# Optimization experiments

Measured on AMD Instinct MI355X. Metric: run time of the kernel, lower is better.

## Reference

```python
import jax, jax.numpy as jnp
import numpy as np

HIDDEN = 768
NUM_HEADS = 12
HEAD_DIM = HIDDEN // NUM_HEADS
BIAS_SCALE = 0.5


def setup_inputs() -> dict:
    key = jax.random.key(0)
    ks = jax.random.split(key, 8)
    B, S = 4, 2048
    s = 1.0 / np.sqrt(HIDDEN)
    return {
        "hidden_states": jax.random.normal(ks[0], (B, S, HIDDEN), dtype=jnp.float32),
        "attention_mask": jnp.ones((B, S), dtype=jnp.float32),
        "Wq": jax.random.normal(ks[1], (HIDDEN, HIDDEN), dtype=jnp.float32) * s,
        "bq": jnp.zeros((HIDDEN,), dtype=jnp.float32),
        "Wk": jax.random.normal(ks[2], (HIDDEN, HIDDEN), dtype=jnp.float32) * s,
        "bk": jnp.zeros((HIDDEN,), dtype=jnp.float32),
        "Wv": jax.random.normal(ks[3], (HIDDEN, HIDDEN), dtype=jnp.float32) * s,
        "bv": jnp.zeros((HIDDEN,), dtype=jnp.float32),
        "head_bias": jnp.full((NUM_HEADS, 1, 1), 0.1, dtype=jnp.float32),
    }


def _split_heads(x):
    # [B,S,H] -> [B,nh,S,hd]
    B, S, _ = x.shape
    return x.reshape(B, S, NUM_HEADS, HEAD_DIM).transpose(0, 2, 1, 3)


def reference(hidden_states, attention_mask, Wq, bq, Wk, bk, Wv, bv, head_bias):
    q = _split_heads(hidden_states @ Wq.T + bq)
    k = _split_heads(hidden_states @ Wk.T + bk)
    v = _split_heads(hidden_states @ Wv.T + bv)
    # [B,nh,S,S]
    scores = jnp.einsum("bhqd,bhkd->bhqk", q, k) / np.sqrt(HEAD_DIM).astype(np.float32)
    scores = scores + BIAS_SCALE * head_bias  # head_bias broadcasts [nh,1,1]
    ext_mask = (1.0 - attention_mask[:, None, None, :]) * -10000.0
    scores = scores + ext_mask
    probs = jax.nn.softmax(scores, axis=-1)  # dropout is identity in eval
    ctx = jnp.einsum("bhqk,bhkd->bhqd", probs, v)
    B, _, S, _ = ctx.shape
    return ctx.transpose(0, 2, 1, 3).reshape(B, S, HIDDEN)
```

## Files before the change

kernel.cpp:

```cpp
#include <hip/hip_runtime.h>

#define LOG2E 1.44269504088896340736f
#define QSCALE 0.18033688011112042f
#define MREF 16.0f

typedef _Float16 half8 __attribute__((ext_vector_type(8)));
typedef _Float16 half4_t __attribute__((ext_vector_type(4)));
typedef __fp16 fp16x2 __attribute__((ext_vector_type(2)));
typedef float f32x4 __attribute__((ext_vector_type(4)));
typedef float f32x16 __attribute__((ext_vector_type(16)));
typedef unsigned int u32x2 __attribute__((ext_vector_type(2)));

__device__ __forceinline__ void gld16(const void* g, void* l) {
  __builtin_amdgcn_global_load_lds(
      (const __attribute__((address_space(1))) void*)g,
      (__attribute__((address_space(3))) void*)l, 16, 0, 0);
}

__global__ void prep_all(const float* __restrict__ hidden, const float* __restrict__ Wq,
                         const float* __restrict__ Wk, const float* __restrict__ Wv,
                         _Float16* __restrict__ hb, _Float16* __restrict__ wqb,
                         _Float16* __restrict__ wkb, _Float16* __restrict__ wvb) {
  const int NH = 1572864, NW = 147456;
  int i = blockIdx.x * blockDim.x + threadIdx.x;
  int st = gridDim.x * blockDim.x;
  for (int idx = i; idx < NH + 3 * NW; idx += st) {
    const float* src; _Float16* dst; int off;
    if (idx < NH) { src = hidden; dst = hb; off = idx; }
    else if (idx < NH + NW) { src = Wq; dst = wqb; off = idx - NH; }
    else if (idx < NH + 2 * NW) { src = Wk; dst = wkb; off = idx - NH - NW; }
    else { src = Wv; dst = wvb; off = idx - NH - 2 * NW; }
    float4 v = reinterpret_cast<const float4*>(src)[off];
    half4_t hh;
    hh[0] = (_Float16)v.x; hh[1] = (_Float16)v.y; hh[2] = (_Float16)v.z; hh[3] = (_Float16)v.w;
    reinterpret_cast<half4_t*>(dst)[off] = hh;
  }
}

__global__ void prep_mask(const float* __restrict__ mask, float* __restrict__ mkb, int n) {
  int i = blockIdx.x * blockDim.x + threadIdx.x;
  if (i < n) mkb[i] = (1.0f - mask[i]) * (-10000.0f * LOG2E) - MREF;
}

__global__ __launch_bounds__(256) void qkv_gemm(
    const _Float16* __restrict__ X,
    const _Float16* __restrict__ Wq, const _Float16* __restrict__ Wk, const _Float16* __restrict__ Wv,
    const float* __restrict__ bq, const float* __restrict__ bk, const float* __restrict__ bv,
    _Float16* __restrict__ qo, _Float16* __restrict__ ko, _Float16* __restrict__ vo) {
  __shared__ _Float16 Al[2][128 * 32];
  __shared__ _Float16 Bl[2][128 * 32];
  const int tid = threadIdx.x;
  const int lane = tid & 63, w = tid >> 6;
  const int wr = w >> 1, wc = w & 1;
  const int mt = blockIdx.x, ntl = blockIdx.y, mode = blockIdx.z;
  const _Float16* W = (mode == 0) ? Wq : (mode == 1) ? Wk : Wv;
  const float* bias = (mode == 0) ? bq : (mode == 1) ? bk : bv;
  _Float16* out = (mode == 0) ? qo : (mode == 1) ? ko : vo;
  const float oscale = (mode == 0) ? QSCALE : 1.0f;

  const _Float16* Xb = X + (size_t)mt * 128 * 768;
  const _Float16* Wb = W + (size_t)ntl * 128 * 768;

  const f32x4 zero4 = {0.f, 0.f, 0.f, 0.f};
  f32x4 acc[4][4];
#pragma unroll
  for (int i = 0; i < 4; ++i)
#pragma unroll
    for (int j = 0; j < 4; ++j) acc[i][j] = zero4;

  auto stage = [&](int bufi, int kt) {
#pragma unroll
    for (int it = 0; it < 2; ++it) {
      int ci = tid + it * 256;
      int row = ci >> 2, c = ci & 3;
      int sw = ((c ^ ((row >> 1) & 3)) << 4);
      gld16((const char*)(Xb + row * 768) + kt * 64 + sw, (char*)&Al[bufi][0] + ci * 16);
      gld16((const char*)(Wb + row * 768) + kt * 64 + sw, (char*)&Bl[bufi][0] + ci * 16);
    }
  };

  stage(0, 0);
  __syncthreads();
  int buf = 0;
  for (int kt = 0; kt < 24; ++kt) {
    if (kt + 1 < 24) stage(buf ^ 1, kt + 1);
    half8 af[4], bf[4];
#pragma unroll
    for (int mi = 0; mi < 4; ++mi) {
      int row = wr * 64 + mi * 16 + (lane & 15);
      int cc = (lane >> 4) ^ ((row >> 1) & 3);
      af[mi] = *(const half8*)((const char*)&Al[buf][0] + row * 64 + cc * 16);
    }
#pragma unroll
    for (int ni = 0; ni < 4; ++ni) {
      int row = wc * 64 + ni * 16 + (lane & 15);
      int cc = (lane >> 4) ^ ((row >> 1) & 3);
      bf[ni] = *(const half8*)((const char*)&Bl[buf][0] + row * 64 + cc * 16);
    }
#pragma unroll
    for (int mi = 0; mi < 4; ++mi)
#pragma unroll
      for (int ni = 0; ni < 4; ++ni)
        acc[mi][ni] = __builtin_amdgcn_mfma_f32_16x16x32_f16(af[mi], bf[ni], acc[mi][ni], 0, 0, 0);
    __syncthreads();
    buf ^= 1;
  }

  const int m0 = mt * 128 + wr * 64, n0 = ntl * 128 + wc * 64;
#pragma unroll
  for (int ni = 0; ni < 4; ++ni) {
    int n = n0 + ni * 16 + (lane & 15);
    float bvv = bias[n];
    int h = n >> 6, d = n & 63;
#pragma unroll
    for (int mi = 0; mi < 4; ++mi) {
      int m = m0 + mi * 16 + ((lane >> 4) << 2);
      int b = m >> 11, s = m & 2047;
      if (mode < 2) {
        _Float16* dst = out + (((size_t)(b * 12 + h) * 2048 + s) * 64 + d);
#pragma unroll
        for (int r = 0; r < 4; ++r) dst[(size_t)r * 64] = (_Float16)((acc[mi][ni][r] + bvv) * oscale);
      } else {
        half4_t pk;
#pragma unroll
        for (int r = 0; r < 4; ++r) pk[r] = (_Float16)(acc[mi][ni][r] + bvv);
        *(half4_t*)(out + ((size_t)(b * 12 + h) * 64 + d) * 2048 + s) = pk;
      }
    }
  }
}

__global__ __launch_bounds__(256) void flash_attn(
    const _Float16* __restrict__ qb, const _Float16* __restrict__ kbuf,
    const _Float16* __restrict__ vtb, const float* __restrict__ mkb,
    float* __restrict__ out) {
  __shared__ _Float16 Kl[2][64 * 64];
  __shared__ _Float16 Vl[2][64 * 64];
  __shared__ float Ml[2048];

  const int tid = threadIdx.x;
  const int lane = tid & 63, w = tid >> 6;
  const int l31 = lane & 31, hi32 = lane >> 5;

  const int i = blockIdx.x;
  const int bh = (i & 7) + 8 * ((i >> 3) >> 4);
  const int qt = (i >> 3) & 15;
  const int b = bh / 12, h = bh % 12;
  const int q0w = qt * 128 + w * 32;

  const _Float16* Kg = kbuf + (size_t)bh * 2048 * 64;
  const _Float16* Vg = vtb + (size_t)bh * 64 * 2048;

  half8 qf[4];
  {
    const _Float16* qp = qb + ((size_t)bh * 2048 + q0w + l31) * 64 + hi32 * 8;
#pragma unroll
    for (int c = 0; c < 4; ++c) qf[c] = *(const half8*)(qp + c * 16);
  }

  auto stageK = [&](int nb, int t) {
#pragma unroll
    for (int it = 0; it < 2; ++it) {
      int ci = tid + it * 256;
      int row = ci >> 3, c = ci & 7;
      int sw = ((c ^ (row & 7)) << 4);
      gld16((const char*)Kg + (size_t)t * 8192 + row * 128 + sw, (char*)&Kl[nb][0] + ci * 16);
    }
  };
  auto stageV = [&](int nb, int t) {
#pragma unroll
    for (int it = 0; it < 2; ++it) {
      int ci = tid + it * 256;
      int row = ci >> 3, c = ci & 7;
      int sw = ((c ^ (row & 7)) << 4);
      gld16((const char*)Vg + (size_t)row * 4096 + t * 128 + sw, (char*)&Vl[nb][0] + ci * 16);
    }
  };

  stageK(0, 0);
  stageV(0, 0);
  {
    const char* ms = (const char*)(mkb + (size_t)b * 2048);
#pragma unroll
    for (int it = 0; it < 2; ++it) {
      int ci = tid + it * 256;
      gld16(ms + ci * 16, (char*)Ml + ci * 16);
    }
  }
  __syncthreads();

  f32x16 o[2], o_sum;
#pragma unroll
  for (int dt = 0; dt < 2; ++dt)
#pragma unroll
    for (int r = 0; r < 16; ++r) o[dt][r] = 0.f;
#pragma unroll
  for (int r = 0; r < 16; ++r) o_sum[r] = 0.f;

  const half8 ones = {(_Float16)1.f, (_Float16)1.f, (_Float16)1.f, (_Float16)1.f,
                      (_Float16)1.f, (_Float16)1.f, (_Float16)1.f, (_Float16)1.f};

  int buf = 0;
  for (int t = 0; t < 32; ++t) {
    if (t + 1 < 32) {
      stageK(buf ^ 1, t + 1);
      stageV(buf ^ 1, t + 1);
    }

    const char* kb = (const char*)&Kl[buf][0];
    const float* mlt = Ml + t * 64 + hi32 * 4;
    f32x16 sc[2];
    __builtin_amdgcn_s_setprio(1);
#pragma unroll
    for (int kt = 0; kt < 2; ++kt) {
      f32x16 z;
#pragma unroll
      for (int g = 0; g < 4; ++g) {
        f32x4 m4 = *(const f32x4*)(mlt + kt * 32 + g * 8);
        z[g * 4 + 0] = m4[0]; z[g * 4 + 1] = m4[1];
        z[g * 4 + 2] = m4[2]; z[g * 4 + 3] = m4[3];
      }
      int row = kt * 32 + l31;
      const char* krow = kb + row * 128;
      int swz = (row & 7) << 4;
#pragma unroll
      for (int c = 0; c < 4; ++c) {
        half8 ka = *(const half8*)(krow + ((c * 32 + hi32 * 16) ^ swz));
        z = __builtin_amdgcn_mfma_f32_32x32x16_f16(ka, qf[c], z, 0, 0, 0);
      }
      sc[kt] = z;
    }
    __builtin_amdgcn_s_setprio(0);

#pragma unroll
    for (int kt = 0; kt < 2; ++kt)
#pragma unroll
      for (int r = 0; r < 16; ++r)
        sc[kt][r] = __builtin_amdgcn_exp2f(sc[kt][r]);

    half8 pa[4];
#pragma unroll
    for (int kt = 0; kt < 2; ++kt)
#pragma unroll
      for (int cc = 0; cc < 2; ++cc) {
        int b0 = cc * 8;
        union { fp16x2 hh; unsigned u; } u01, u23, u45, u67;
        u01.hh = __builtin_amdgcn_cvt_pkrtz(sc[kt][b0 + 0], sc[kt][b0 + 1]);
        u23.hh = __builtin_amdgcn_cvt_pkrtz(sc[kt][b0 + 2], sc[kt][b0 + 3]);
        u45.hh = __builtin_amdgcn_cvt_pkrtz(sc[kt][b0 + 4], sc[kt][b0 + 5]);
        u67.hh = __builtin_amdgcn_cvt_pkrtz(sc[kt][b0 + 6], sc[kt][b0 + 7]);
        u32x2 s1 = __builtin_amdgcn_permlane32_swap(u01.u, u45.u, false, false);
        u32x2 s2 = __builtin_amdgcn_permlane32_swap(u23.u, u67.u, false, false);
        union { unsigned u[4]; half8 hv; } a;
        a.u[0] = s1[0]; a.u[1] = s2[0]; a.u[2] = s1[1]; a.u[3] = s2[1];
        pa[kt * 2 + cc] = a.hv;
      }

    const char* vb = (const char*)&Vl[buf][0];
    __builtin_amdgcn_s_setprio(1);
#pragma unroll
    for (int dt = 0; dt < 2; ++dt) {
      int row = dt * 32 + l31;
      const char* vrow = vb + row * 128;
      int swz = (row & 7) << 4;
#pragma unroll
      for (int ch = 0; ch < 4; ++ch) {
        half8 vbf = *(const half8*)(vrow + ((ch * 32 + hi32 * 16) ^ swz));
        o[dt] = __builtin_amdgcn_mfma_f32_32x32x16_f16(pa[ch], vbf, o[dt], 0, 0, 0);
      }
    }
#pragma unroll
    for (int ch = 0; ch < 4; ++ch)
      o_sum = __builtin_amdgcn_mfma_f32_32x32x16_f16(pa[ch], ones, o_sum, 0, 0, 0);
    __builtin_amdgcn_s_setprio(0);

    __syncthreads();
    buf ^= 1;
  }

#pragma unroll
  for (int r = 0; r < 16; ++r) {
    int qrow = (r & 3) + 8 * (r >> 2) + 4 * hi32;
    float iq = 1.f / o_sum[r];
    float* op = out + ((size_t)(b * 2048) + q0w + qrow) * 768 + h * 64 + l31;
    op[0] = o[0][r] * iq;
    op[32] = o[1][r] * iq;
  }
}

extern "C" void kernel_launch(void* const* d_in, const int* in_sizes, int n_in,
                              void* d_out, int out_size, void* d_ws, size_t ws_size,
                              hipStream_t stream) {
  const float* hidden = (const float*)d_in[0];
  const float* mask = (const float*)d_in[1];
  const float* Wq = (const float*)d_in[2];
  const float* bq = (const float*)d_in[3];
  const float* Wk = (const float*)d_in[4];
  const float* bk = (const float*)d_in[5];
  const float* Wv = (const float*)d_in[6];
  const float* bv = (const float*)d_in[7];
  float* out = (float*)d_out;

  char* ws = (char*)d_ws;
  _Float16* hb   = (_Float16*)(ws);
  _Float16* wqb  = (_Float16*)(ws + 12582912);
  _Float16* wkb  = (_Float16*)(ws + 13762560);
  _Float16* wvb  = (_Float16*)(ws + 14942208);
  _Float16* qbuf = (_Float16*)(ws + 16121856);
  _Float16* kbuf = (_Float16*)(ws + 28704768);
  _Float16* vtb  = (_Float16*)(ws + 41287680);
  float* mkb     = (float*)(ws);

  prep_all<<<dim3(2048), dim3(256), 0, stream>>>(hidden, Wq, Wk, Wv, hb, wqb, wkb, wvb);
  qkv_gemm<<<dim3(64, 6, 3), dim3(256), 0, stream>>>(hb, wqb, wkb, wvb, bq, bk, bv,
                                                     qbuf, kbuf, vtb);
  prep_mask<<<dim3(32), dim3(256), 0, stream>>>(mask, mkb, 8192);
  flash_attn<<<dim3(768), dim3(256), 0, stream>>>(qbuf, kbuf, vtb, mkb, out);
}
```

Baseline: 149.8 us.

## Add mask via rank-1 MFMA and stagger KV tile order across blocks

Replaces the fp32 mask staged in LDS with an fp16 mask read directly from global memory. The mask is added to the scores through an extra rank-1 MFMA, which removes the LDS mask buffer and the per-tile vector loads that initialised the accumulators. It also rotates the starting KV tile per block (phase from the block index mod 3) to spread memory traffic across blocks. The cost is one extra MFMA per score tile, fp16 rounding of the mask offsets (near -16), and per-tile scalar global loads.

```diff
diff --git a/kernel.cpp b/kernel.cpp
--- a/kernel.cpp
+++ b/kernel.cpp
@@ -37,9 +37,9 @@
   }
 }
 
-__global__ void prep_mask(const float* __restrict__ mask, float* __restrict__ mkb, int n) {
+__global__ void prep_mask16(const float* __restrict__ mask, _Float16* __restrict__ mk16, int n) {
   int i = blockIdx.x * blockDim.x + threadIdx.x;
-  if (i < n) mkb[i] = (1.0f - mask[i]) * (-10000.0f * LOG2E) - MREF;
+  if (i < n) mk16[i] = (_Float16)((1.0f - mask[i]) * (-10000.0f * LOG2E) - MREF);
 }
 
 __global__ __launch_bounds__(256) void qkv_gemm(
@@ -132,11 +132,10 @@
 
 __global__ __launch_bounds__(256) void flash_attn(
     const _Float16* __restrict__ qb, const _Float16* __restrict__ kbuf,
-    const _Float16* __restrict__ vtb, const float* __restrict__ mkb,
+    const _Float16* __restrict__ vtb, const _Float16* __restrict__ mk16,
     float* __restrict__ out) {
   __shared__ _Float16 Kl[2][64 * 64];
   __shared__ _Float16 Vl[2][64 * 64];
-  __shared__ float Ml[2048];
 
   const int tid = threadIdx.x;
   const int lane = tid & 63, w = tid >> 6;
@@ -150,6 +149,7 @@
 
   const _Float16* Kg = kbuf + (size_t)bh * 2048 * 64;
   const _Float16* Vg = vtb + (size_t)bh * 64 * 2048;
+  const _Float16* mkrow = mk16 + (size_t)b * 2048;
 
   half8 qf[4];
   {
@@ -177,57 +177,57 @@
     }
   };
 
-  stageK(0, 0);
-  stageV(0, 0);
-  {
-    const char* ms = (const char*)(mkb + (size_t)b * 2048);
-#pragma unroll
-    for (int it = 0; it < 2; ++it) {
-      int ci = tid + it * 256;
-      gld16(ms + ci * 16, (char*)Ml + ci * 16);
-    }
-  }
-  __syncthreads();
-
-  f32x16 o[2], o_sum;
-#pragma unroll
-  for (int dt = 0; dt < 2; ++dt)
-#pragma unroll
-    for (int r = 0; r < 16; ++r) o[dt][r] = 0.f;
-#pragma unroll
-  for (int r = 0; r < 16; ++r) o_sum[r] = 0.f;
-
+  f32x16 zero16;
+#pragma unroll
+  for (int r = 0; r < 16; ++r) zero16[r] = 0.f;
+  half8 b4 = {};
+  b4[0] = (hi32 == 0) ? (_Float16)1.f : (_Float16)0.f;
   const half8 ones = {(_Float16)1.f, (_Float16)1.f, (_Float16)1.f, (_Float16)1.f,
                       (_Float16)1.f, (_Float16)1.f, (_Float16)1.f, (_Float16)1.f};
 
+  const int phase = (i % 3) * 11;
+
+  stageK(0, phase);
+  stageV(0, phase);
+  __syncthreads();
+
+  f32x16 o[2], o_sum;
+#pragma unroll
+  for (int dt = 0; dt < 2; ++dt)
+#pragma unroll
+    for (int r = 0; r < 16; ++r) o[dt][r] = 0.f;
+#pragma unroll
+  for (int r = 0; r < 16; ++r) o_sum[r] = 0.f;
+
   int buf = 0;
   for (int t = 0; t < 32; ++t) {
+    const int tc = (phase + t) & 31;
     if (t + 1 < 32) {
-      stageK(buf ^ 1, t + 1);
-      stageV(buf ^ 1, t + 1);
-    }
+      const int tn = (phase + t + 1) & 31;
+      stageK(buf ^ 1, tn);
+      stageV(buf ^ 1, tn);
+    }
+
+    _Float16 mv0 = mkrow[tc * 64 + l31];
+    _Float16 mv1 = mkrow[tc * 64 + 32 + l31];
 
     const char* kb = (const char*)&Kl[buf][0];
-    const float* mlt = Ml + t * 64 + hi32 * 4;
     f32x16 sc[2];
     __builtin_amdgcn_s_setprio(1);
 #pragma unroll
     for (int kt = 0; kt < 2; ++kt) {
-      f32x16 z;
-#pragma unroll
-      for (int g = 0; g < 4; ++g) {
-        f32x4 m4 = *(const f32x4*)(mlt + kt * 32 + g * 8);
-        z[g * 4 + 0] = m4[0]; z[g * 4 + 1] = m4[1];
-        z[g * 4 + 2] = m4[2]; z[g * 4 + 3] = m4[3];
-      }
       int row = kt * 32 + l31;
       const char* krow = kb + row * 128;
       int swz = (row & 7) << 4;
+      f32x16 z = zero16;
 #pragma unroll
       for (int c = 0; c < 4; ++c) {
         half8 ka = *(const half8*)(krow + ((c * 32 + hi32 * 16) ^ swz));
         z = __builtin_amdgcn_mfma_f32_32x32x16_f16(ka, qf[c], z, 0, 0, 0);
       }
+      half8 a4 = {};
+      a4[0] = (hi32 == 0) ? (kt == 0 ? mv0 : mv1) : (_Float16)0.f;
+      z = __builtin_amdgcn_mfma_f32_32x32x16_f16(a4, b4, z, 0, 0, 0);
       sc[kt] = z;
     }
     __builtin_amdgcn_s_setprio(0);
@@ -309,11 +309,11 @@
   _Float16* qbuf = (_Float16*)(ws + 16121856);
   _Float16* kbuf = (_Float16*)(ws + 28704768);
   _Float16* vtb  = (_Float16*)(ws + 41287680);
-  float* mkb     = (float*)(ws);
+  _Float16* mk16 = (_Float16*)(ws);
 
   prep_all<<<dim3(2048), dim3(256), 0, stream>>>(hidden, Wq, Wk, Wv, hb, wqb, wkb, wvb);
   qkv_gemm<<<dim3(64, 6, 3), dim3(256), 0, stream>>>(hb, wqb, wkb, wvb, bq, bk, bv,
                                                      qbuf, kbuf, vtb);
-  prep_mask<<<dim3(32), dim3(256), 0, stream>>>(mask, mkb, 8192);
-  flash_attn<<<dim3(768), dim3(256), 0, stream>>>(qbuf, kbuf, vtb, mkb, out);
-}
+  prep_mask16<<<dim3(32), dim3(256), 0, stream>>>(mask, mk16, 8192);
+  flash_attn<<<dim3(768), dim3(256), 0, stream>>>(qbuf, kbuf, vtb, mk16, out);
+}
```

After: 145.7 us. -2.7%, faster.
